# Kernel tuning notes

Measured on AMD Instinct MI355X. Metric: run time of the kernel, lower is better.

The kernel has to match this reference:

```python
import jax, jax.numpy as jnp
import numpy as np

N, E, NC = 50000, 800000, 5
H, C = 4, 16      # branch GATConvs: heads=4, out=16 -> 64
H2, C2 = 4, 32    # conv2/conv3: heads=4, out=32 -> 128
HID = 128


def _gat(x, src, dst, W, a_s, a_d, b, mask=None, edge_attr=None, We=None, a_e=None):
    """PyG-style GATConv with add_self_loops=True (fill_value='mean' for edge_attr)."""
    n = x.shape[0]
    h, c = a_s.shape
    hx = (x @ W).reshape(n, h, c)                      # [N,H,C]
    as_n = (hx * a_s).sum(-1)                          # [N,H]
    ad_n = (hx * a_d).sum(-1)                          # [N,H]
    alpha = as_n[src] + ad_n[dst]                      # [E,H]
    loop = as_n + ad_n                                 # self-loop scores [N,H]
    if edge_attr is not None:
        ee = (edge_attr @ We).reshape(-1, h, c)        # [E,H,C]
        alpha = alpha + (ee * a_e).sum(-1)
        w = mask.astype(x.dtype) if mask is not None else jnp.ones((edge_attr.shape[0],), x.dtype)
        # fill_value='mean': self-loop attr = mean of (masked) incoming edge_attr
        loop_attr = jax.ops.segment_sum(edge_attr * w[:, None], dst, n) / \
                    jnp.maximum(jax.ops.segment_sum(w, dst, n), 1.0)[:, None]
        loop = loop + ((loop_attr @ We).reshape(n, h, c) * a_e).sum(-1)
    alpha = jax.nn.leaky_relu(alpha, 0.2)
    loop = jax.nn.leaky_relu(loop, 0.2)
    if mask is not None:
        alpha = jnp.where(mask[:, None], alpha, -jnp.inf)
    # segment softmax over destination neighborhoods (self-loop always present)
    m = jnp.maximum(jax.ops.segment_max(alpha, dst, n), loop)      # [N,H], finite
    ex = jnp.exp(alpha - m[dst])                                   # [E,H]
    if mask is not None:
        ex = jnp.where(mask[:, None], ex, 0.0)
    exl = jnp.exp(loop - m)                                        # [N,H]
    denom = jax.ops.segment_sum(ex, dst, n) + exl
    out = jax.ops.segment_sum(ex[:, :, None] * hx[src], dst, n) + exl[:, :, None] * hx
    return (out / denom[:, :, None]).reshape(n, h * c) + b


def setup_inputs() -> dict:
    key = jax.random.key(0)
    ks = iter(jax.random.split(key, 64))
    def nrm(shape, s=0.1):
        return jax.random.normal(next(ks), shape, jnp.float32) * s
    d = {}
    d["x"] = nrm((N, 1), 1.0)
    d["edge_index"] = jax.random.randint(next(ks), (2, E), 0, N, jnp.int32)
    d["edge_attr"] = nrm((E, 3), 1.0)
    d["mask_t"] = jax.random.randint(next(ks), (E,), 0, 2, jnp.int32).astype(bool)
    d["mask_g"] = jax.random.randint(next(ks), (E,), 0, 2, jnp.int32).astype(bool)
    d["mask_p"] = jax.random.randint(next(ks), (E,), 0, 2, jnp.int32).astype(bool)
    for p in ("t", "g", "p"):
        d[f"W{p}"] = nrm((1, H * C))
        d[f"a{p}s"] = nrm((H, C)); d[f"a{p}d"] = nrm((H, C)); d[f"a{p}e"] = nrm((H, C))
        d[f"W{p}e"] = nrm((3, H * C))
        d[f"b{p}"] = jnp.zeros((H * C,), jnp.float32)
    d["Wf"] = nrm((3 * H * C, HID)); d["bf"] = jnp.zeros((HID,), jnp.float32)
    d["W2"] = nrm((HID, H2 * C2)); d["a2s"] = nrm((H2, C2)); d["a2d"] = nrm((H2, C2)); d["b2"] = jnp.zeros((H2 * C2,), jnp.float32)
    d["W3"] = nrm((HID, H2 * C2)); d["a3s"] = nrm((H2, C2)); d["a3d"] = nrm((H2, C2)); d["b3"] = jnp.zeros((H2 * C2,), jnp.float32)
    d["Wc1"] = nrm((HID, HID // 2)); d["bc1"] = jnp.zeros((HID // 2,), jnp.float32)
    d["Wc2"] = nrm((HID // 2, NC)); d["bc2"] = jnp.zeros((NC,), jnp.float32)
    return d


def reference(x, edge_index, edge_attr, mask_t, mask_g, mask_p,
              Wt, ats, atd, ate, Wte, bt,
              Wg, ags, agd, age, Wge, bg,
              Wp, aps, apd, ape, Wpe, bp,
              Wf, bf, W2, a2s, a2d, b2, W3, a3s, a3d, b3,
              Wc1, bc1, Wc2, bc2):
    src, dst = edge_index[0], edge_index[1]
    ht = _gat(x, src, dst, Wt, ats, atd, bt, mask_t, edge_attr, Wte, ate)
    hg = _gat(x, src, dst, Wg, ags, agd, bg, mask_g, edge_attr, Wge, age)
    hp = _gat(x, src, dst, Wp, aps, apd, bp, mask_p, edge_attr, Wpe, ape)
    h = jax.nn.relu(jnp.concatenate([ht, hg, hp], -1) @ Wf + bf)
    h = jax.nn.relu(_gat(h, src, dst, W2, a2s, a2d, b2))
    h = jax.nn.relu(_gat(h, src, dst, W3, a3s, a3d, b3))
    logits = jax.nn.relu(h @ Wc1 + bc1) @ Wc2 + bc2
    return jax.nn.log_softmax(logits, -1)
```

## Files before the change

### kernel.cpp

```cpp
#include <hip/hip_runtime.h>
#include <hip/hip_bf16.h>

#define LEAKY(v) ((v) > 0.f ? (v) : 0.2f * (v))

typedef __attribute__((ext_vector_type(8))) short s8;
typedef __attribute__((ext_vector_type(4))) float f4;
typedef __attribute__((ext_vector_type(4))) unsigned short us4;

__device__ __forceinline__ unsigned short f_to_bf16(float f) {
    union { float f; unsigned int i; } v; v.f = f;
    unsigned int x = v.i;
    return (unsigned short)((x + 0x7fffu + ((x >> 16) & 1u)) >> 16);
}

__device__ __forceinline__ float2 bf2_to_f2(unsigned int u) {
    union { unsigned int i; float f; } a, b;
    a.i = (u & 0xffffu) << 16;
    b.i = u & 0xffff0000u;
    float2 r; r.x = a.f; r.y = b.f;
    return r;
}

struct ConstBuf {
    float ws[3][4];
    float wd[3][4];
    float M[3][3][4];
    float G[12][128];
    float bias2[128];
};
#define CB_FLOATS 1724

struct BranchW { const float *W, *as_, *ad_, *ae, *We, *b; };
struct PreArgs { BranchW br[3]; const float *Wf, *bf; ConstBuf* cb; };

__global__ void k_pre_all(PreArgs A, const float* __restrict__ W2, unsigned short* __restrict__ wf2,
                          const float* __restrict__ W3, unsigned short* __restrict__ wf3,
                          const float* __restrict__ Wc1, unsigned short* __restrict__ wc1f,
                          int* __restrict__ deg, int N) {
    int t = threadIdx.x;
    if (blockIdx.x == 0) {
        if (t < 24) {
            int b = t / 8, r = t % 8, h = r & 3; bool isd = r >= 4;
            const float* a = isd ? A.br[b].ad_ : A.br[b].as_;
            float s = 0.f;
            for (int c = 0; c < 16; ++c) s += A.br[b].W[h * 16 + c] * a[h * 16 + c];
            if (isd) A.cb->wd[b][h] = s; else A.cb->ws[b][h] = s;
        }
        if (t >= 32 && t < 68) {
            int id = t - 32, b = id / 12, k = (id % 12) / 4, h = id & 3;
            float s = 0.f;
            for (int c = 0; c < 16; ++c) s += A.br[b].We[k * 64 + h * 16 + c] * A.br[b].ae[h * 16 + c];
            A.cb->M[b][k][h] = s;
        }
        if (t >= 128) {
            int j = t - 128;
            float s = A.bf[j];
            for (int b = 0; b < 3; ++b)
                for (int i = 0; i < 64; ++i)
                    s += A.br[b].b[i] * A.Wf[(b * 64 + i) * 128 + j];
            A.cb->bias2[(j & 7) * 16 + (j >> 3)] = s;
        }
        for (int id = t; id < 1536; id += 256) {
            int r = id >> 7, j = id & 127, b = r >> 2, h = r & 3;
            float s = 0.f;
            for (int c = 0; c < 16; ++c)
                s += A.br[b].W[h * 16 + c] * A.Wf[(b * 64 + h * 16 + c) * 128 + j];
            A.cb->G[r][(j & 7) * 16 + (j >> 3)] = s;
        }
    } else if (blockIdx.x <= 2) {
        const float* W = (blockIdx.x == 1) ? W2 : W3;
        unsigned short* out = (blockIdx.x == 1) ? wf2 : wf3;
        for (int i = t; i < 16384; i += 256) {
            int j = i & 7, lane = (i >> 3) & 63, kk = (i >> 9) & 3, ct = i >> 11;
            int k = kk * 32 + (lane >> 4) * 8 + j;
            int n = ct * 16 + (lane & 15);
            out[i] = f_to_bf16(W[k * 128 + n]);
        }
    } else if (blockIdx.x == 3) {
        for (int i = t; i < 8192; i += 256) {
            int j = i & 7, lane = (i >> 3) & 63, kk = (i >> 9) & 3, ct = i >> 11;
            int k = kk * 32 + (lane >> 4) * 8 + j;
            int col = ct * 16 + (lane & 15);
            wc1f[i] = f_to_bf16(Wc1[k * 64 + col]);
        }
    } else {
        int idx = (blockIdx.x - 4) * 256 + t;
        if (idx < N) deg[idx] = 0;
    }
}

__global__ void k_count(const int* __restrict__ ei, int E, int* __restrict__ deg) {
    int e = blockIdx.x * blockDim.x + threadIdx.x;
    if (e < E) atomicAdd(&deg[__builtin_nontemporal_load(ei + E + e)], 1);
}

#define SCAN_EPB 2048

__global__ void k_scan1(const int* __restrict__ deg, int* __restrict__ off,
                        int* __restrict__ partials, int total) {
    __shared__ int sd[256];
    int t = threadIdx.x;
    int base = blockIdx.x * SCAN_EPB + t * 8;
    int v[8];
    int s = 0;
    #pragma unroll
    for (int i = 0; i < 8; ++i) {
        int idx = base + i;
        v[i] = (idx < total - 1) ? deg[idx] : 0;
        s += v[i];
    }
    sd[t] = s;
    __syncthreads();
    #pragma unroll
    for (int ofs = 1; ofs < 256; ofs <<= 1) {
        int u = (t >= ofs) ? sd[t - ofs] : 0;
        __syncthreads();
        sd[t] += u;
        __syncthreads();
    }
    if (t == 255) partials[blockIdx.x] = sd[255];
    int run = sd[t] - s;
    #pragma unroll
    for (int i = 0; i < 8; ++i) {
        int idx = base + i;
        if (idx < total) off[idx] = run;
        run += v[i];
    }
}

__global__ void k_scan3(int* __restrict__ off, const int* __restrict__ partials,
                        int* __restrict__ cursor, int total) {
    int idx = blockIdx.x * blockDim.x + threadIdx.x;
    if (idx < total) {
        int pb = idx / SCAN_EPB;
        int addv = 0;
        for (int j = 0; j < pb; ++j) addv += partials[j];
        int v = off[idx] + addv;
        off[idx] = v;
        if (idx < total - 1) cursor[idx] = v;
    }
}

__global__ void k_scatter(const int* __restrict__ ei, const float* __restrict__ attr,
                          const int* __restrict__ mt, const int* __restrict__ mg,
                          const int* __restrict__ mp, int E, int chunk,
                          int* __restrict__ cursor, float4* __restrict__ rec) {
    int r = blockIdx.x & 7;
    int slice = blockIdx.x >> 3;
    int e = slice * 256 + threadIdx.x;
    if (e >= E) return;
    int d = __builtin_nontemporal_load(ei + E + e);
    if ((unsigned)(d - r * chunk) >= (unsigned)chunk) return;
    int p = atomicAdd(&cursor[d], 1);
    float4 rr;
    rr.x = __builtin_nontemporal_load(attr + e * 3 + 0);
    rr.y = __builtin_nontemporal_load(attr + e * 3 + 1);
    rr.z = __builtin_nontemporal_load(attr + e * 3 + 2);
    int mtv = __builtin_nontemporal_load(mt + e);
    int mgv = __builtin_nontemporal_load(mg + e);
    int mpv = __builtin_nontemporal_load(mp + e);
    int srcv = __builtin_nontemporal_load(ei + e);
    unsigned int bits = (mtv != 0 ? 1u : 0u) | (mgv != 0 ? 2u : 0u) | (mpv != 0 ? 4u : 0u);
    rr.w = __int_as_float((int)((unsigned)srcv | (bits << 16)));
    rec[p] = rr;
}

__global__ void k_branch(const float* __restrict__ x, const int* __restrict__ off,
                         const float4* __restrict__ rec, int* __restrict__ csr_src,
                         const ConstBuf* __restrict__ cb, unsigned short* __restrict__ h1, int N) {
    __shared__ float sc[CB_FLOATS];
    for (int i = threadIdx.x; i < CB_FLOATS; i += 256) sc[i] = ((const float*)cb)[i];
    __syncthreads();
    int g = threadIdx.x >> 4, l = threadIdx.x & 15;
    int n = blockIdx.x * 16 + g;
    if (n >= N) return;

    float num[12], den[12], asum[9], cnt[3];
    #pragma unroll
    for (int i = 0; i < 12; ++i) { num[i] = 0.f; den[i] = 0.f; }
    #pragma unroll
    for (int i = 0; i < 9; ++i) asum[i] = 0.f;
    cnt[0] = cnt[1] = cnt[2] = 0.f;

    float xn = x[n];
    int beg = off[n], end = off[n + 1];
    for (int p = beg + l; p < end; p += 16) {
        float4 r = rec[p];
        unsigned int packed = (unsigned int)__float_as_int(r.w);
        int src = (int)(packed & 0xffffu);
        unsigned int bits = packed >> 16;
        csr_src[p] = src;
        float xs = x[src];
        float a0 = r.x, a1 = r.y, a2 = r.z;
        #pragma unroll
        for (int b = 0; b < 3; ++b) {
            if ((bits >> b) & 1u) {
                cnt[b] += 1.f;
                asum[b * 3 + 0] += a0; asum[b * 3 + 1] += a1; asum[b * 3 + 2] += a2;
                #pragma unroll
                for (int h = 0; h < 4; ++h) {
                    float al = xs * sc[b * 4 + h] + xn * sc[12 + b * 4 + h]
                             + a0 * sc[24 + b * 12 + 0 + h]
                             + a1 * sc[24 + b * 12 + 4 + h]
                             + a2 * sc[24 + b * 12 + 8 + h];
                    al = LEAKY(al);
                    float ex = __expf(al);
                    den[b * 4 + h] += ex;
                    num[b * 4 + h] += ex * xs;
                }
            }
        }
    }
    #pragma unroll
    for (int m = 1; m < 16; m <<= 1) {
        #pragma unroll
        for (int i = 0; i < 12; ++i) {
            num[i] += __shfl_xor(num[i], m, 64);
            den[i] += __shfl_xor(den[i], m, 64);
        }
        #pragma unroll
        for (int i = 0; i < 9; ++i) asum[i] += __shfl_xor(asum[i], m, 64);
        #pragma unroll
        for (int i = 0; i < 3; ++i) cnt[i] += __shfl_xor(cnt[i], m, 64);
    }
    float S[12];
    #pragma unroll
    for (int b = 0; b < 3; ++b) {
        float inv = 1.f / fmaxf(cnt[b], 1.f);
        float l0 = asum[b * 3 + 0] * inv, l1 = asum[b * 3 + 1] * inv, l2 = asum[b * 3 + 2] * inv;
        #pragma unroll
        for (int h = 0; h < 4; ++h) {
            float lp = xn * (sc[b * 4 + h] + sc[12 + b * 4 + h])
                     + l0 * sc[24 + b * 12 + 0 + h]
                     + l1 * sc[24 + b * 12 + 4 + h]
                     + l2 * sc[24 + b * 12 + 8 + h];
            lp = LEAKY(lp);
            float exl = __expf(lp);
            float sden = den[b * 4 + h] + exl;
            S[b * 4 + h] = (num[b * 4 + h] + exl * xn) / sden;
        }
    }
    int jb = l * 8;
    unsigned int o[4];
    #pragma unroll
    for (int q2 = 0; q2 < 4; ++q2) {
        float v0, v1;
        #pragma unroll
        for (int s = 0; s < 2; ++s) {
            int q = q2 * 2 + s;
            float a = sc[60 + 1536 + q * 16 + l];
            #pragma unroll
            for (int k = 0; k < 12; ++k) a += S[k] * sc[60 + k * 128 + q * 16 + l];
            if (s == 0) v0 = fmaxf(a, 0.f); else v1 = fmaxf(a, 0.f);
        }
        o[q2] = (unsigned int)f_to_bf16(v0) | ((unsigned int)f_to_bf16(v1) << 16);
    }
    uint4 pack; pack.x = o[0]; pack.y = o[1]; pack.z = o[2]; pack.w = o[3];
    *(uint4*)(h1 + (size_t)n * 128 + jb) = pack;
}

__global__ void k_mm128b(const unsigned short* __restrict__ A, const unsigned short* __restrict__ wf,
                         const float* __restrict__ a_s, const float* __restrict__ a_d,
                         unsigned short* __restrict__ hxb, float* __restrict__ as_,
                         float* __restrict__ ad_, int N) {
    __shared__ unsigned short sA[64 * 136];
    __shared__ unsigned short sW[16384];
    int tid = threadIdx.x;
    int base = blockIdx.x * 64;
    const float4* wf4 = (const float4*)wf;
    float4* sW4 = (float4*)sW;
    #pragma unroll
    for (int i = 0; i < 8; ++i) sW4[tid + i * 256] = wf4[tid + i * 256];
    #pragma unroll
    for (int i = 0; i < 4; ++i) {
        int f = tid + i * 256;
        int row = f >> 4, c8 = f & 15;
        int n = base + row;
        uint4 v = (n < N) ? ((const uint4*)A)[(size_t)n * 16 + c8]
                          : make_uint4(0u, 0u, 0u, 0u);
        *(uint4*)(&sA[row * 136 + c8 * 8]) = v;
    }
    __syncthreads();
    int wv = tid >> 6, lane = tid & 63;
    int q = lane >> 4, l15 = lane & 15;
    int rowbase = wv * 16;
    s8 af[4];
    #pragma unroll
    for (int kk = 0; kk < 4; ++kk)
        af[kk] = *(const s8*)(&sA[(rowbase + l15) * 136 + kk * 32 + q * 8]);
    float as8[8], ad8[8];
    #pragma unroll
    for (int ct = 0; ct < 8; ++ct) { as8[ct] = a_s[ct * 16 + l15]; ad8[ct] = a_d[ct * 16 + l15]; }
    float ss[4][4], sdd[4][4];
    #pragma unroll
    for (int r = 0; r < 4; ++r)
        #pragma unroll
        for (int hh = 0; hh < 4; ++hh) { ss[r][hh] = 0.f; sdd[r][hh] = 0.f; }
    #pragma unroll
    for (int ct = 0; ct < 8; ++ct) {
        f4 acc = {0.f, 0.f, 0.f, 0.f};
        #pragma unroll
        for (int kk = 0; kk < 4; ++kk) {
            s8 bfr = *(const s8*)(&sW[((ct * 4 + kk) * 64 + lane) * 8]);
            acc = __builtin_amdgcn_mfma_f32_16x16x32_bf16(af[kk], bfr, acc, 0, 0, 0);
        }
        int hh = ct >> 1;
        float asv = as8[ct], adv = ad8[ct];
        #pragma unroll
        for (int r = 0; r < 4; ++r) {
            int n = base + rowbase + q * 4 + r;
            if (n < N) hxb[(size_t)n * 128 + ct * 16 + l15] = f_to_bf16(acc[r]);
            ss[r][hh] += acc[r] * asv;
            sdd[r][hh] += acc[r] * adv;
        }
    }
    #pragma unroll
    for (int m = 1; m < 16; m <<= 1) {
        #pragma unroll
        for (int r = 0; r < 4; ++r)
            #pragma unroll
            for (int hh = 0; hh < 4; ++hh) {
                ss[r][hh] += __shfl_xor(ss[r][hh], m, 64);
                sdd[r][hh] += __shfl_xor(sdd[r][hh], m, 64);
            }
    }
    #pragma unroll
    for (int hh = 0; hh < 4; ++hh) {
        if (l15 == hh) {
            #pragma unroll
            for (int r = 0; r < 4; ++r) {
                int n = base + rowbase + q * 4 + r;
                if (n < N) {
                    as_[(size_t)n * 4 + hh] = ss[r][hh];
                    ad_[(size_t)n * 4 + hh] = sdd[r][hh];
                }
            }
        }
    }
}

__global__ void k_gatagg(const unsigned short* __restrict__ hxb, const float* __restrict__ as_,
                         const float* __restrict__ ad_, const float* __restrict__ b,
                         const int* __restrict__ off, const int* __restrict__ csr_src,
                         unsigned short* __restrict__ out, int N) {
    int wave = threadIdx.x >> 6, lane = threadIdx.x & 63;
    int n = blockIdx.x * 4 + wave;
    if (n >= N) return;
    int h = lane >> 4;
    int lofs = lane * 2;
    int hm = lane & 3;
    int im = lane >> 2;
    float adn = ad_[(size_t)n * 4 + h];
    float adnm = ad_[(size_t)n * 4 + hm];
    int beg = off[n], end = off[n + 1];
    float acc0 = 0.f, acc1 = 0.f, accd = 0.f;
    for (int p = beg; p < end; p += 16) {
        int pm = p + im;
        bool vm = pm < end;
        int sm = csr_src[vm ? pm : beg];
        float em = as_[(size_t)sm * 4 + hm];
        float exm = vm ? __expf(LEAKY(em + adnm)) : 0.f;
        #pragma unroll
        for (int i = 0; i < 16; ++i) {
            int sb = __shfl(sm, i * 4, 64);
            float ex = __shfl(exm, i * 4 + h, 64);
            unsigned int u = *(const unsigned int*)(hxb + (size_t)sb * 128 + lofs);
            float2 v = bf2_to_f2(u);
            acc0 += ex * v.x; acc1 += ex * v.y; accd += ex;
        }
    }
    float aln = LEAKY(as_[(size_t)n * 4 + h] + adn);
    float exl = __expf(aln);
    unsigned int un = *(const unsigned int*)(hxb + (size_t)n * 128 + lofs);
    float2 vn = bf2_to_f2(un);
    float inv = 1.f / (accd + exl);
    float o0 = fmaxf((acc0 + exl * vn.x) * inv + b[lofs + 0], 0.f);
    float o1 = fmaxf((acc1 + exl * vn.y) * inv + b[lofs + 1], 0.f);
    unsigned int pk = (unsigned int)f_to_bf16(o0) | ((unsigned int)f_to_bf16(o1) << 16);
    *(unsigned int*)(out + (size_t)n * 128 + lofs) = pk;
}

__global__ void k_cls(const unsigned short* __restrict__ h3, const unsigned short* __restrict__ wc1f,
                      const float* __restrict__ bc1, const float* __restrict__ Wc2,
                      const float* __restrict__ bc2, float* __restrict__ out, int N) {
    __shared__ unsigned short sA[64 * 136];
    __shared__ unsigned short sW[8192];
    int tid = threadIdx.x;
    int base = blockIdx.x * 64;
    const float4* wf4 = (const float4*)wc1f;
    float4* sW4 = (float4*)sW;
    #pragma unroll
    for (int i = 0; i < 4; ++i) sW4[tid + i * 256] = wf4[tid + i * 256];
    #pragma unroll
    for (int i = 0; i < 4; ++i) {
        int f = tid + i * 256;
        int row = f >> 4, c8 = f & 15;
        int n = base + row;
        uint4 v = (n < N) ? ((const uint4*)h3)[(size_t)n * 16 + c8]
                          : make_uint4(0u, 0u, 0u, 0u);
        *(uint4*)(&sA[row * 136 + c8 * 8]) = v;
    }
    __syncthreads();
    int wv = tid >> 6, lane = tid & 63;
    int q = lane >> 4, l15 = lane & 15;
    int rowbase = wv * 16;
    s8 af[4];
    #pragma unroll
    for (int kk = 0; kk < 4; ++kk)
        af[kk] = *(const s8*)(&sA[(rowbase + l15) * 136 + kk * 32 + q * 8]);
    float p[4][5];
    #pragma unroll
    for (int r = 0; r < 4; ++r)
        #pragma unroll
        for (int c = 0; c < 5; ++c) p[r][c] = 0.f;
    #pragma unroll
    for (int ct = 0; ct < 4; ++ct) {
        f4 acc = {0.f, 0.f, 0.f, 0.f};
        #pragma unroll
        for (int kk = 0; kk < 4; ++kk) {
            s8 bfr = *(const s8*)(&sW[((ct * 4 + kk) * 64 + lane) * 8]);
            acc = __builtin_amdgcn_mfma_f32_16x16x32_bf16(af[kk], bfr, acc, 0, 0, 0);
        }
        int col = ct * 16 + l15;
        float bcv = bc1[col];
        float w2v[5];
        #pragma unroll
        for (int c = 0; c < 5; ++c) w2v[c] = Wc2[col * 5 + c];
        #pragma unroll
        for (int r = 0; r < 4; ++r) {
            float t = fmaxf(acc[r] + bcv, 0.f);
            #pragma unroll
            for (int c = 0; c < 5; ++c) p[r][c] += t * w2v[c];
        }
    }
    #pragma unroll
    for (int m = 1; m < 16; m <<= 1) {
        #pragma unroll
        for (int r = 0; r < 4; ++r)
            #pragma unroll
            for (int c = 0; c < 5; ++c)
                p[r][c] += __shfl_xor(p[r][c], m, 64);
    }
    if (l15 == 0) {
        #pragma unroll
        for (int r = 0; r < 4; ++r) {
            int n = base + rowbase + q * 4 + r;
            if (n >= N) continue;
            float l[5], mx = -1e30f;
            #pragma unroll
            for (int c = 0; c < 5; ++c) { l[c] = p[r][c] + bc2[c]; mx = fmaxf(mx, l[c]); }
            float s = 0.f;
            #pragma unroll
            for (int c = 0; c < 5; ++c) s += __expf(l[c] - mx);
            float lse = mx + __logf(s);
            #pragma unroll
            for (int c = 0; c < 5; ++c) out[(size_t)n * 5 + c] = l[c] - lse;
        }
    }
}

extern "C" void kernel_launch(void* const* d_in, const int* in_sizes, int n_in,
                              void* d_out, int out_size, void* d_ws, size_t ws_size,
                              hipStream_t stream) {
    const float* x    = (const float*)d_in[0];
    const int*   ei   = (const int*)d_in[1];
    const float* attr = (const float*)d_in[2];
    const int*   mt   = (const int*)d_in[3];
    const int*   mg   = (const int*)d_in[4];
    const int*   mp   = (const int*)d_in[5];
    const float* Wf   = (const float*)d_in[24];
    const float* bf   = (const float*)d_in[25];
    const float* W2   = (const float*)d_in[26];
    const float* a2s  = (const float*)d_in[27];
    const float* a2d  = (const float*)d_in[28];
    const float* b2   = (const float*)d_in[29];
    const float* W3   = (const float*)d_in[30];
    const float* a3s  = (const float*)d_in[31];
    const float* a3d  = (const float*)d_in[32];
    const float* b3   = (const float*)d_in[33];
    const float* Wc1  = (const float*)d_in[34];
    const float* bc1  = (const float*)d_in[35];
    const float* Wc2  = (const float*)d_in[36];
    const float* bc2  = (const float*)d_in[37];

    int N = in_sizes[0];
    int E = in_sizes[1] / 2;

    char* w = (char*)d_ws;
    auto alloc = [&](size_t bytes) {
        char* p = w;
        w += (bytes + 255) & ~(size_t)255;
        return p;
    };
    int* off      = (int*)alloc((size_t)(N + 1) * 4);
    int* cursor   = (int*)alloc((size_t)N * 4);
    int* deg      = (int*)alloc((size_t)N * 4);
    int* partials = (int*)alloc(1024 * 4);
    int* csr_src  = (int*)alloc((size_t)E * 4);
    ConstBuf* cb  = (ConstBuf*)alloc(sizeof(ConstBuf));
    float* as_    = (float*)alloc((size_t)N * 4 * 4);
    float* ad_    = (float*)alloc((size_t)N * 4 * 4);
    unsigned short* xb = (unsigned short*)alloc((size_t)N * 256);
    float4* rec   = (float4*)alloc((size_t)E * 16);
    unsigned short* hxb = (unsigned short*)alloc((size_t)N * 256);
    unsigned short* wf2 = (unsigned short*)alloc(16384 * 2);
    unsigned short* wf3 = (unsigned short*)alloc(16384 * 2);
    unsigned short* wc1f = (unsigned short*)alloc(8192 * 2);

    PreArgs pa;
    for (int b = 0; b < 3; ++b) {
        pa.br[b].W   = (const float*)d_in[6 + b * 6 + 0];
        pa.br[b].as_ = (const float*)d_in[6 + b * 6 + 1];
        pa.br[b].ad_ = (const float*)d_in[6 + b * 6 + 2];
        pa.br[b].ae  = (const float*)d_in[6 + b * 6 + 3];
        pa.br[b].We  = (const float*)d_in[6 + b * 6 + 4];
        pa.br[b].b   = (const float*)d_in[6 + b * 6 + 5];
    }
    pa.Wf = Wf; pa.bf = bf; pa.cb = cb;

    int total = N + 1;
    int nScanBlocks = (total + SCAN_EPB - 1) / SCAN_EPB;

    hipLaunchKernelGGL(k_pre_all, dim3(4 + (N + 255) / 256), dim3(256), 0, stream,
                       pa, W2, wf2, W3, wf3, Wc1, wc1f, deg, N);
    int gE = (E + 255) / 256;
    hipLaunchKernelGGL(k_count, dim3(gE), dim3(256), 0, stream, ei, E, deg);
    hipLaunchKernelGGL(k_scan1, dim3(nScanBlocks), dim3(256), 0, stream, deg, off, partials, total);
    hipLaunchKernelGGL(k_scan3, dim3((total + 255) / 256), dim3(256), 0, stream,
                       off, partials, cursor, total);
    int chunk = (N + 7) / 8;
    hipLaunchKernelGGL(k_scatter, dim3(gE * 8), dim3(256), 0, stream,
                       ei, attr, mt, mg, mp, E, chunk, cursor, rec);
    hipLaunchKernelGGL(k_branch, dim3((N + 15) / 16), dim3(256), 0, stream,
                       x, off, rec, csr_src, cb, xb, N);
    hipLaunchKernelGGL(k_mm128b, dim3((N + 63) / 64), dim3(256), 0, stream,
                       xb, wf2, a2s, a2d, hxb, as_, ad_, N);
    hipLaunchKernelGGL(k_gatagg, dim3((N + 3) / 4), dim3(256), 0, stream,
                       hxb, as_, ad_, b2, off, csr_src, xb, N);
    hipLaunchKernelGGL(k_mm128b, dim3((N + 63) / 64), dim3(256), 0, stream,
                       xb, wf3, a3s, a3d, hxb, as_, ad_, N);
    hipLaunchKernelGGL(k_gatagg, dim3((N + 3) / 4), dim3(256), 0, stream,
                       hxb, as_, ad_, b3, off, csr_src, xb, N);
    hipLaunchKernelGGL(k_cls, dim3((N + 63) / 64), dim3(256), 0, stream,
                       xb, wc1f, bc1, Wc2, bc2, (float*)d_out, N);
}
```

Before: 413.6 us.

## Pre-bucket edges by destination range before CSR scatter

Replaces the eight-pass scatter, where every block re-read all destination indices and kept only its own range, with two kernels. The first makes one pass over the edges, packs each record with its 16-bit destination and groups them into eight destination-range buckets using wave ballots and one atomic per bucket per block. The second reads only its own bucket's records and does the cursor atomics plus record writes. This removes the repeated index reads and early exits, at the cost of an extra launch and an intermediate buffer that is written and read back. It assumes node ids fit in 16 bits and that no bucket exceeds its fixed capacity. Non-temporal loads are also dropped from the degree count.

```diff
diff --git a/kernel.cpp b/kernel.cpp
--- a/kernel.cpp
+++ b/kernel.cpp
@@ -36,7 +36,7 @@
 __global__ void k_pre_all(PreArgs A, const float* __restrict__ W2, unsigned short* __restrict__ wf2,
                           const float* __restrict__ W3, unsigned short* __restrict__ wf3,
                           const float* __restrict__ Wc1, unsigned short* __restrict__ wc1f,
-                          int* __restrict__ deg, int N) {
+                          int* __restrict__ deg, int* __restrict__ bucketCount, int N) {
     int t = threadIdx.x;
     if (blockIdx.x == 0) {
         if (t < 24) {
@@ -52,6 +52,7 @@
             for (int c = 0; c < 16; ++c) s += A.br[b].We[k * 64 + h * 16 + c] * A.br[b].ae[h * 16 + c];
             A.cb->M[b][k][h] = s;
         }
+        if (t >= 68 && t < 76) bucketCount[t - 68] = 0;
         if (t >= 128) {
             int j = t - 128;
             float s = A.bf[j];
@@ -91,7 +92,7 @@
 
 __global__ void k_count(const int* __restrict__ ei, int E, int* __restrict__ deg) {
     int e = blockIdx.x * blockDim.x + threadIdx.x;
-    if (e < E) atomicAdd(&deg[__builtin_nontemporal_load(ei + E + e)], 1);
+    if (e < E) atomicAdd(&deg[ei[E + e]], 1);
 }
 
 #define SCAN_EPB 2048
@@ -141,27 +142,61 @@
     }
 }
 
-__global__ void k_scatter(const int* __restrict__ ei, const float* __restrict__ attr,
-                          const int* __restrict__ mt, const int* __restrict__ mg,
-                          const int* __restrict__ mp, int E, int chunk,
-                          int* __restrict__ cursor, float4* __restrict__ rec) {
+__global__ void k_bucket(const int* __restrict__ ei, const float* __restrict__ attr,
+                         const int* __restrict__ mt, const int* __restrict__ mg,
+                         const int* __restrict__ mp, int E, int chunk, int capB,
+                         int* __restrict__ bucketCount, float4* __restrict__ brec,
+                         unsigned short* __restrict__ bdst) {
+    __shared__ int wcnt[4][8];
+    __shared__ int wbase[4][8];
+    __shared__ int gbase[8];
+    int tid = threadIdx.x, wv = tid >> 6, lane = tid & 63;
+    int e = blockIdx.x * 256 + tid;
+    int r = -1, d = 0, s = 0;
+    float a0 = 0.f, a1 = 0.f, a2 = 0.f;
+    unsigned int bits = 0;
+    if (e < E) {
+        d = ei[E + e]; s = ei[e];
+        a0 = attr[e * 3 + 0]; a1 = attr[e * 3 + 1]; a2 = attr[e * 3 + 2];
+        bits = (mt[e] != 0 ? 1u : 0u) | (mg[e] != 0 ? 2u : 0u) | (mp[e] != 0 ? 4u : 0u);
+        r = d / chunk; if (r > 7) r = 7;
+    }
+    int rank = 0;
+    #pragma unroll
+    for (int k = 0; k < 8; ++k) {
+        unsigned long long m = __ballot(r == k);
+        if (r == k) rank = (int)__popcll(m & ((1ull << lane) - 1ull));
+        if (lane == 0) wcnt[wv][k] = (int)__popcll(m);
+    }
+    __syncthreads();
+    if (tid < 8) {
+        int c0 = wcnt[0][tid], c1 = wcnt[1][tid], c2 = wcnt[2][tid], c3 = wcnt[3][tid];
+        wbase[0][tid] = 0; wbase[1][tid] = c0; wbase[2][tid] = c0 + c1; wbase[3][tid] = c0 + c1 + c2;
+        gbase[tid] = atomicAdd(&bucketCount[tid], c0 + c1 + c2 + c3);
+    }
+    __syncthreads();
+    if (r >= 0) {
+        int pos = gbase[r] + wbase[wv][r] + rank;
+        if (pos < capB) {
+            size_t idx = (size_t)r * capB + pos;
+            brec[idx] = make_float4(a0, a1, a2,
+                __int_as_float((int)((unsigned)s | (bits << 16))));
+            bdst[idx] = (unsigned short)d;
+        }
+    }
+}
+
+__global__ void k_scatter2(const float4* __restrict__ brec, const unsigned short* __restrict__ bdst,
+                           const int* __restrict__ bucketCount, int capB,
+                           int* __restrict__ cursor, float4* __restrict__ rec) {
     int r = blockIdx.x & 7;
     int slice = blockIdx.x >> 3;
-    int e = slice * 256 + threadIdx.x;
-    if (e >= E) return;
-    int d = __builtin_nontemporal_load(ei + E + e);
-    if ((unsigned)(d - r * chunk) >= (unsigned)chunk) return;
+    int i = slice * 256 + threadIdx.x;
+    if (i >= bucketCount[r]) return;
+    size_t idx = (size_t)r * capB + i;
+    float4 rr = brec[idx];
+    int d = bdst[idx];
     int p = atomicAdd(&cursor[d], 1);
-    float4 rr;
-    rr.x = __builtin_nontemporal_load(attr + e * 3 + 0);
-    rr.y = __builtin_nontemporal_load(attr + e * 3 + 1);
-    rr.z = __builtin_nontemporal_load(attr + e * 3 + 2);
-    int mtv = __builtin_nontemporal_load(mt + e);
-    int mgv = __builtin_nontemporal_load(mg + e);
-    int mpv = __builtin_nontemporal_load(mp + e);
-    int srcv = __builtin_nontemporal_load(ei + e);
-    unsigned int bits = (mtv != 0 ? 1u : 0u) | (mgv != 0 ? 2u : 0u) | (mpv != 0 ? 4u : 0u);
-    rr.w = __int_as_float((int)((unsigned)srcv | (bits << 16)));
     rec[p] = rr;
 }
 
@@ -496,6 +531,7 @@
     int* cursor   = (int*)alloc((size_t)N * 4);
     int* deg      = (int*)alloc((size_t)N * 4);
     int* partials = (int*)alloc(1024 * 4);
+    int* bucketCount = (int*)alloc(8 * 4);
     int* csr_src  = (int*)alloc((size_t)E * 4);
     ConstBuf* cb  = (ConstBuf*)alloc(sizeof(ConstBuf));
     float* as_    = (float*)alloc((size_t)N * 4 * 4);
@@ -506,6 +542,9 @@
     unsigned short* wf2 = (unsigned short*)alloc(16384 * 2);
     unsigned short* wf3 = (unsigned short*)alloc(16384 * 2);
     unsigned short* wc1f = (unsigned short*)alloc(8192 * 2);
+    int capB = (E + 7) / 8 + 65536;
+    float4* brec  = (float4*)alloc((size_t)8 * capB * 16);
+    unsigned short* bdst = (unsigned short*)alloc((size_t)8 * capB * 2);
 
     PreArgs pa;
     for (int b = 0; b < 3; ++b) {
@@ -522,15 +561,17 @@
     int nScanBlocks = (total + SCAN_EPB - 1) / SCAN_EPB;
 
     hipLaunchKernelGGL(k_pre_all, dim3(4 + (N + 255) / 256), dim3(256), 0, stream,
-                       pa, W2, wf2, W3, wf3, Wc1, wc1f, deg, N);
+                       pa, W2, wf2, W3, wf3, Wc1, wc1f, deg, bucketCount, N);
     int gE = (E + 255) / 256;
     hipLaunchKernelGGL(k_count, dim3(gE), dim3(256), 0, stream, ei, E, deg);
     hipLaunchKernelGGL(k_scan1, dim3(nScanBlocks), dim3(256), 0, stream, deg, off, partials, total);
     hipLaunchKernelGGL(k_scan3, dim3((total + 255) / 256), dim3(256), 0, stream,
                        off, partials, cursor, total);
     int chunk = (N + 7) / 8;
-    hipLaunchKernelGGL(k_scatter, dim3(gE * 8), dim3(256), 0, stream,
-                       ei, attr, mt, mg, mp, E, chunk, cursor, rec);
+    hipLaunchKernelGGL(k_bucket, dim3(gE), dim3(256), 0, stream,
+                       ei, attr, mt, mg, mp, E, chunk, capB, bucketCount, brec, bdst);
+    hipLaunchKernelGGL(k_scatter2, dim3(gE * 8), dim3(256), 0, stream,
+                       brec, bdst, bucketCount, capB, cursor, rec);
     hipLaunchKernelGGL(k_branch, dim3((N + 15) / 16), dim3(256), 0, stream,
                        x, off, rec, csr_src, cb, xb, N);
     hipLaunchKernelGGL(k_mm128b, dim3((N + 63) / 64), dim3(256), 0, stream,
```

After: 441.9 us. +6.8%, slower.
